# Optimization experiments

Measured on AMD Instinct MI355X. Metric: run time of the kernel, lower is better.

## Reference

```python
import jax, jax.numpy as jnp
import numpy as np

INV_SQRT2 = 0.7071067811865476  # 1/sqrt(2), haar analysis/synthesis filter value
J = 3  # decomp_level


def _haar_dwt(x, J):
    """x: [B, H, L] with L divisible by 2**J. Returns (ca, [cd_1..cd_J])."""
    cds = []
    for _ in range(J):
        a = x[..., 0::2]
        b = x[..., 1::2]
        cds.append((a - b) * INV_SQRT2)  # detail (high-freq)
        x = (a + b) * INV_SQRT2          # approximation (low-freq)
    return x, cds


def _haar_idwt(ca, cds):
    """Inverse of _haar_dwt; cds ordered coarse-last as produced above."""
    for cd in reversed(cds):
        even = (ca + cd) * INV_SQRT2
        odd = (ca - cd) * INV_SQRT2
        ca = jnp.stack([even, odd], axis=-1).reshape(ca.shape[:-1] + (ca.shape[-1] * 2,))
    return ca


def setup_inputs() -> dict:
    key = jax.random.key(0)
    ks = jax.random.split(key, 6)
    B, S, H = 64, 512, 1024
    return {
        "input_tensor": jax.random.normal(ks[0], (B, S, H), dtype=jnp.float32),
        "ww0": jax.random.uniform(ks[1], (256, H), dtype=jnp.float32),
        "ww1": jax.random.uniform(ks[2], (128, H), dtype=jnp.float32),
        "ww2": jax.random.uniform(ks[3], (64, H), dtype=jnp.float32),
        "srt": jax.random.uniform(ks[4], (H,), dtype=jnp.float32),
        "sqrt_beta": jax.random.normal(ks[5], (1, 1, H), dtype=jnp.float32),
        "ln_weight": jnp.ones((H,), dtype=jnp.float32),
        "ln_bias": jnp.zeros((H,), dtype=jnp.float32),
    }


def reference(input_tensor, ww0, ww1, ww2, srt, sqrt_beta, ln_weight, ln_bias):
    # DWT over the sequence axis: operate on [B, H, L]
    x_bhl = jnp.transpose(input_tensor, (0, 2, 1))
    ca, cds = _haar_dwt(x_bhl, J)
    # HighFrequencySignalScale: cd_i *= ww_i * srt^2 (ww_i is [L_i, H], cd is [B, H, L_i])
    s2 = srt ** 2  # [H]
    scaled = [cd * jnp.transpose(w * s2)[None] for cd, w in zip(cds, (ww0, ww1, ww2))]
    low_pass = jnp.transpose(_haar_idwt(ca, scaled), (0, 2, 1))  # [B, S, H]
    high_pass = input_tensor - low_pass
    seq_emb = low_pass + (sqrt_beta ** 2) * high_pass  # not_restore=False branch
    # dropout is identity at inference; residual + TF-style LayerNorm
    x = seq_emb + input_tensor
    u = jnp.mean(x, axis=-1, keepdims=True)
    s = jnp.mean((x - u) ** 2, axis=-1, keepdims=True)
    return ln_weight * (x - u) / jnp.sqrt(s + 1e-12) + ln_bias
```

## Files before the change

kernel.cpp:

```cpp
#include <hip/hip_runtime.h>

typedef float f4 __attribute__((ext_vector_type(4)));

#define INV_SQRT2 0.70710678118654752440f

__global__ __launch_bounds__(256) void freq_layer_fused(
    const float* __restrict__ in,
    const float* __restrict__ ww0,
    const float* __restrict__ ww1,
    const float* __restrict__ ww2,
    const float* __restrict__ srt,
    const float* __restrict__ sqrt_beta,
    const float* __restrict__ ln_w,
    const float* __restrict__ ln_b,
    float* __restrict__ out)
{
    constexpr int H = 1024;
    constexpr int S = 512;
    constexpr float c = INV_SQRT2;

    const int t  = threadIdx.x;
    const int k  = blockIdx.x & 63;
    const int b  = blockIdx.x >> 6;
    const int h0 = t << 2;

    const size_t rowbase = ((size_t)b * S + (size_t)(k << 3)) * H + (size_t)h0;

    f4 y[8];
    #pragma unroll
    for (int j = 0; j < 8; ++j)
        y[j] = *reinterpret_cast<const f4*>(in + rowbase + (size_t)j * H);

    f4 s2 = *reinterpret_cast<const f4*>(srt + h0);
    s2 *= s2;
    f4 b2 = *reinterpret_cast<const f4*>(sqrt_beta + h0);
    b2 *= b2;

    f4 w0[4], w1[2], w2v;
    #pragma unroll
    for (int j = 0; j < 4; ++j)
        w0[j] = *reinterpret_cast<const f4*>(ww0 + (size_t)((k << 2) + j) * H + h0) * s2;
    #pragma unroll
    for (int j = 0; j < 2; ++j)
        w1[j] = *reinterpret_cast<const f4*>(ww1 + (size_t)((k << 1) + j) * H + h0) * s2;
    w2v = *reinterpret_cast<const f4*>(ww2 + (size_t)k * H + h0) * s2;

    float ssum[8], ssq[8];
    #pragma unroll
    for (int j = 0; j < 8; ++j) { ssum[j] = 0.f; ssq[j] = 0.f; }

    #pragma unroll
    for (int hh = 0; hh < 4; ++hh) {
        float yc[8];
        #pragma unroll
        for (int j = 0; j < 8; ++j) yc[j] = y[j][hh];

        const float a0 = (yc[0] + yc[1]) * c;
        const float a1 = (yc[2] + yc[3]) * c;
        const float a2 = (yc[4] + yc[5]) * c;
        const float a3 = (yc[6] + yc[7]) * c;
        const float d10 = (yc[0] - yc[1]) * c * w0[0][hh];
        const float d11 = (yc[2] - yc[3]) * c * w0[1][hh];
        const float d12 = (yc[4] - yc[5]) * c * w0[2][hh];
        const float d13 = (yc[6] - yc[7]) * c * w0[3][hh];
        const float bb0 = (a0 + a1) * c;
        const float bb1 = (a2 + a3) * c;
        const float d20 = (a0 - a1) * c * w1[0][hh];
        const float d21 = (a2 - a3) * c * w1[1][hh];
        const float cc  = (bb0 + bb1) * c;
        const float d3  = (bb0 - bb1) * c * w2v[hh];

        const float b0p = (cc + d3) * c;
        const float b1p = (cc - d3) * c;
        const float a0p = (b0p + d20) * c;
        const float a1p = (b0p - d20) * c;
        const float a2p = (b1p + d21) * c;
        const float a3p = (b1p - d21) * c;
        float lp[8];
        lp[0] = (a0p + d10) * c;
        lp[1] = (a0p - d10) * c;
        lp[2] = (a1p + d11) * c;
        lp[3] = (a1p - d11) * c;
        lp[4] = (a2p + d12) * c;
        lp[5] = (a2p - d12) * c;
        lp[6] = (a3p + d13) * c;
        lp[7] = (a3p - d13) * c;

        const float bb = b2[hh];
        #pragma unroll
        for (int j = 0; j < 8; ++j) {
            const float hpv = yc[j] - lp[j];
            const float v   = lp[j] + bb * hpv + yc[j];
            y[j][hh] = v;
            ssum[j] += v;
            ssq[j]  += v * v;
        }
    }

    #pragma unroll
    for (int m = 1; m < 64; m <<= 1) {
        #pragma unroll
        for (int j = 0; j < 8; ++j) {
            ssum[j] += __shfl_xor(ssum[j], m, 64);
            ssq[j]  += __shfl_xor(ssq[j],  m, 64);
        }
    }

    __shared__ float red[4][16];
    const int wave = t >> 6;
    if ((t & 63) == 0) {
        #pragma unroll
        for (int j = 0; j < 8; ++j) {
            red[wave][j]     = ssum[j];
            red[wave][8 + j] = ssq[j];
        }
    }
    __syncthreads();

    const f4 lw = *reinterpret_cast<const f4*>(ln_w + h0);
    const f4 lb = *reinterpret_cast<const f4*>(ln_b + h0);

    #pragma unroll
    for (int j = 0; j < 8; ++j) {
        const float Sj = red[0][j] + red[1][j] + red[2][j] + red[3][j];
        const float Qj = red[0][8 + j] + red[1][8 + j] + red[2][8 + j] + red[3][8 + j];
        const float u   = Sj * (1.0f / 1024.0f);
        const float var = Qj * (1.0f / 1024.0f) - u * u;
        const float r   = rsqrtf(var + 1e-12f);
        f4 o;
        #pragma unroll
        for (int hh = 0; hh < 4; ++hh)
            o[hh] = lw[hh] * ((y[j][hh] - u) * r) + lb[hh];
        *reinterpret_cast<f4*>(out + rowbase + (size_t)j * H) = o;
    }
}

extern "C" void kernel_launch(void* const* d_in, const int* in_sizes, int n_in,
                              void* d_out, int out_size, void* d_ws, size_t ws_size,
                              hipStream_t stream) {
    const float* in   = (const float*)d_in[0];
    const float* ww0  = (const float*)d_in[1];
    const float* ww1  = (const float*)d_in[2];
    const float* ww2  = (const float*)d_in[3];
    const float* srt  = (const float*)d_in[4];
    const float* sb   = (const float*)d_in[5];
    const float* lnw  = (const float*)d_in[6];
    const float* lnb  = (const float*)d_in[7];
    float* out = (float*)d_out;

    freq_layer_fused<<<dim3(64 * 64), dim3(256), 0, stream>>>(
        in, ww0, ww1, ww2, srt, sb, lnw, lnb, out);
}
```

Baseline: 47.09 us.

## Process two batches per block and use a transpose-style butterfly reduction

Each block now handles the same 8-row tile for two batch indices (g and g+32), so the ww/srt/beta weight loads are reused across both tiles and the grid is halved. The per-row sum and sum-of-squares reduction is replaced by a recursive-halving butterfly where lanes exchange halves of their 32 accumulators. This cuts the shuffle count from 16 per step to far fewer in total, and a small group of threads then computes mean and rstd into shared memory. In exchange, register pressure roughly doubles because 16 f4 values are live per thread, which may lower occupancy, and the halved grid gives fewer blocks per CU to hide memory latency.

Result: slower. 80.13 us (+70.1%).

```diff
diff --git a/kernel.cpp b/kernel.cpp
--- a/kernel.cpp
+++ b/kernel.cpp
@@ -1,54 +1,14 @@
 #include <hip/hip_runtime.h>
 
 typedef float f4 __attribute__((ext_vector_type(4)));
+typedef float f2 __attribute__((ext_vector_type(2)));
 
 #define INV_SQRT2 0.70710678118654752440f
 
-__global__ __launch_bounds__(256) void freq_layer_fused(
-    const float* __restrict__ in,
-    const float* __restrict__ ww0,
-    const float* __restrict__ ww1,
-    const float* __restrict__ ww2,
-    const float* __restrict__ srt,
-    const float* __restrict__ sqrt_beta,
-    const float* __restrict__ ln_w,
-    const float* __restrict__ ln_b,
-    float* __restrict__ out)
-{
-    constexpr int H = 1024;
-    constexpr int S = 512;
+__device__ __forceinline__ void haar_tile(f4 (&y)[8], const f4 (&w0)[4],
+                                          const f4 (&w1)[2], const f4 w2v,
+                                          const f4 b2, float* vv) {
     constexpr float c = INV_SQRT2;
-
-    const int t  = threadIdx.x;
-    const int k  = blockIdx.x & 63;
-    const int b  = blockIdx.x >> 6;
-    const int h0 = t << 2;
-
-    const size_t rowbase = ((size_t)b * S + (size_t)(k << 3)) * H + (size_t)h0;
-
-    f4 y[8];
-    #pragma unroll
-    for (int j = 0; j < 8; ++j)
-        y[j] = *reinterpret_cast<const f4*>(in + rowbase + (size_t)j * H);
-
-    f4 s2 = *reinterpret_cast<const f4*>(srt + h0);
-    s2 *= s2;
-    f4 b2 = *reinterpret_cast<const f4*>(sqrt_beta + h0);
-    b2 *= b2;
-
-    f4 w0[4], w1[2], w2v;
-    #pragma unroll
-    for (int j = 0; j < 4; ++j)
-        w0[j] = *reinterpret_cast<const f4*>(ww0 + (size_t)((k << 2) + j) * H + h0) * s2;
-    #pragma unroll
-    for (int j = 0; j < 2; ++j)
-        w1[j] = *reinterpret_cast<const f4*>(ww1 + (size_t)((k << 1) + j) * H + h0) * s2;
-    w2v = *reinterpret_cast<const f4*>(ww2 + (size_t)k * H + h0) * s2;
-
-    float ssum[8], ssq[8];
-    #pragma unroll
-    for (int j = 0; j < 8; ++j) { ssum[j] = 0.f; ssq[j] = 0.f; }
-
     #pragma unroll
     for (int hh = 0; hh < 4; ++hh) {
         float yc[8];
@@ -91,29 +51,97 @@
         for (int j = 0; j < 8; ++j) {
             const float hpv = yc[j] - lp[j];
             const float v   = lp[j] + bb * hpv + yc[j];
-            y[j][hh] = v;
-            ssum[j] += v;
-            ssq[j]  += v * v;
+            y[j][hh]   = v;
+            vv[j * 2]     += v;
+            vv[j * 2 + 1] += v * v;
         }
     }
+}
+
+__global__ __launch_bounds__(256) void freq_layer_fused(
+    const float* __restrict__ in,
+    const float* __restrict__ ww0,
+    const float* __restrict__ ww1,
+    const float* __restrict__ ww2,
+    const float* __restrict__ srt,
+    const float* __restrict__ sqrt_beta,
+    const float* __restrict__ ln_w,
+    const float* __restrict__ ln_b,
+    float* __restrict__ out)
+{
+    constexpr int H = 1024;
+    constexpr int S = 512;
+
+    const int t  = threadIdx.x;
+    const int k  = blockIdx.x & 63;
+    const int g  = blockIdx.x >> 6;
+    const int h0 = t << 2;
+
+    const size_t baseA = ((size_t)g * S        + (size_t)(k << 3)) * H + (size_t)h0;
+    const size_t baseB = ((size_t)(g + 32) * S + (size_t)(k << 3)) * H + (size_t)h0;
+
+    f4 yA[8], yB[8];
+    #pragma unroll
+    for (int j = 0; j < 8; ++j)
+        yA[j] = *reinterpret_cast<const f4*>(in + baseA + (size_t)j * H);
+    #pragma unroll
+    for (int j = 0; j < 8; ++j)
+        yB[j] = *reinterpret_cast<const f4*>(in + baseB + (size_t)j * H);
+
+    f4 s2 = *reinterpret_cast<const f4*>(srt + h0);
+    s2 *= s2;
+    f4 b2 = *reinterpret_cast<const f4*>(sqrt_beta + h0);
+    b2 *= b2;
+
+    f4 w0[4], w1[2], w2v;
+    #pragma unroll
+    for (int j = 0; j < 4; ++j)
+        w0[j] = *reinterpret_cast<const f4*>(ww0 + (size_t)((k << 2) + j) * H + h0) * s2;
+    #pragma unroll
+    for (int j = 0; j < 2; ++j)
+        w1[j] = *reinterpret_cast<const f4*>(ww1 + (size_t)((k << 1) + j) * H + h0) * s2;
+    w2v = *reinterpret_cast<const f4*>(ww2 + (size_t)k * H + h0) * s2;
+
+    float v[32];
+    #pragma unroll
+    for (int i = 0; i < 32; ++i) v[i] = 0.f;
+
+    haar_tile(yA, w0, w1, w2v, b2, v);
+    haar_tile(yB, w0, w1, w2v, b2, v + 16);
 
     #pragma unroll
-    for (int m = 1; m < 64; m <<= 1) {
+    for (int r = 0; r < 5; ++r) {
+        const int m    = 1 << r;
+        const int half = 16 >> r;
+        const bool hi  = (t & m) != 0;
         #pragma unroll
-        for (int j = 0; j < 8; ++j) {
-            ssum[j] += __shfl_xor(ssum[j], m, 64);
-            ssq[j]  += __shfl_xor(ssq[j],  m, 64);
+        for (int i = 0; i < half; ++i) {
+            const float send = hi ? v[i] : v[half + i];
+            const float recv = __shfl_xor(send, m, 64);
+            v[i] = (hi ? v[half + i] : v[i]) + recv;
         }
     }
+    v[0] += __shfl_xor(v[0], 32, 64);
 
-    __shared__ float red[4][16];
+    const int l5  = t & 31;
+    const int idx = ((l5 & 1) << 4) | ((l5 & 2) << 2) | (l5 & 4) |
+                    ((l5 & 8) >> 2) | ((l5 & 16) >> 4);
+
+    __shared__ float red[4][32];
+    __shared__ __align__(16) float stats[32];
     const int wave = t >> 6;
-    if ((t & 63) == 0) {
-        #pragma unroll
-        for (int j = 0; j < 8; ++j) {
-            red[wave][j]     = ssum[j];
-            red[wave][8 + j] = ssq[j];
-        }
+    if ((t & 32) == 0) red[wave][idx] = v[0];
+    __syncthreads();
+
+    if (t < 16) {
+        const float s = red[0][2 * t]     + red[1][2 * t] +
+                        red[2][2 * t]     + red[3][2 * t];
+        const float q = red[0][2 * t + 1] + red[1][2 * t + 1] +
+                        red[2][2 * t + 1] + red[3][2 * t + 1];
+        const float u   = s * (1.0f / 1024.0f);
+        const float var = q * (1.0f / 1024.0f) - u * u;
+        stats[2 * t]     = u;
+        stats[2 * t + 1] = rsqrtf(var + 1e-12f);
     }
     __syncthreads();
 
@@ -122,16 +150,21 @@
 
     #pragma unroll
     for (int j = 0; j < 8; ++j) {
-        const float Sj = red[0][j] + red[1][j] + red[2][j] + red[3][j];
-        const float Qj = red[0][8 + j] + red[1][8 + j] + red[2][8 + j] + red[3][8 + j];
-        const float u   = Sj * (1.0f / 1024.0f);
-        const float var = Qj * (1.0f / 1024.0f) - u * u;
-        const float r   = rsqrtf(var + 1e-12f);
+        const f2 st = *reinterpret_cast<const f2*>(&stats[2 * j]);
         f4 o;
         #pragma unroll
         for (int hh = 0; hh < 4; ++hh)
-            o[hh] = lw[hh] * ((y[j][hh] - u) * r) + lb[hh];
-        *reinterpret_cast<f4*>(out + rowbase + (size_t)j * H) = o;
+            o[hh] = lw[hh] * ((yA[j][hh] - st[0]) * st[1]) + lb[hh];
+        *reinterpret_cast<f4*>(out + baseA + (size_t)j * H) = o;
+    }
+    #pragma unroll
+    for (int j = 0; j < 8; ++j) {
+        const f2 st = *reinterpret_cast<const f2*>(&stats[16 + 2 * j]);
+        f4 o;
+        #pragma unroll
+        for (int hh = 0; hh < 4; ++hh)
+            o[hh] = lw[hh] * ((yB[j][hh] - st[0]) * st[1]) + lb[hh];
+        *reinterpret_cast<f4*>(out + baseB + (size_t)j * H) = o;
     }
 }
 
@@ -148,6 +181,6 @@
     const float* lnb  = (const float*)d_in[7];
     float* out = (float*)d_out;
 
-    freq_layer_fused<<<dim3(64 * 64), dim3(256), 0, stream>>>(
+    freq_layer_fused<<<dim3(64 * 32), dim3(256), 0, stream>>>(
         in, ww0, ww1, ww2, srt, sb, lnw, lnb, out);
 }
```
